# Performance work log

Hardware: AMD Instinct MI355X
Metric: run time of the kernel (lower is better)

Reference implementation:

```python
import jax, jax.numpy as jnp
import numpy as np

T, B, I, H = 4096, 2048, 1, 10


def setup_inputs() -> dict:
    key = jax.random.key(0)
    ks = jax.random.split(key, 8)
    k = 1.0 / np.sqrt(H)  # torch default init bound for RNN and Linear(10,1)
    u = lambda kk, shape: jax.random.uniform(kk, shape, jnp.float32, -k, k)
    return {
        "x": jax.random.normal(ks[0], (T, B, I), jnp.float32),
        "h": jnp.zeros((1, B, H), jnp.float32),
        "W_ih": u(ks[1], (H, I)),
        "b_ih": u(ks[2], (H,)),
        "W_hh": u(ks[3], (H, H)),
        "b_hh": u(ks[4], (H,)),
        "W_out": u(ks[5], (1, H)),
        "b_out": u(ks[6], (1,)),
    }


def reference(x, h, W_ih, b_ih, W_hh, b_hh, W_out, b_out):
    # Vanilla RNN: h_t = tanh(x_t @ W_ih^T + b_ih + h_{t-1} @ W_hh^T + b_hh)
    b = b_ih + b_hh  # fuse the two biases once

    def step(h_prev, x_t):  # h_prev: [B,H], x_t: [B,I]
        h_new = jnp.tanh(x_t @ W_ih.T + h_prev @ W_hh.T + b)
        return h_new, h_new

    h_last, ys = jax.lax.scan(step, h[0], x)  # ys: [T,B,H]
    out = ys @ W_out.T + b_out  # [T,B,1]
    return out, h_last[None]  # h: [1,B,H]
```

## Files before the change

### kernel.cpp

```cpp
#include <hip/hip_runtime.h>

#define T_STEPS 4096
#define BATCH   2048
#define HID     10
#define UB      16

__device__ __forceinline__ void issue16(float (&xr)[UB], const float* base) {
#pragma unroll
    for (int u = 0; u < UB; ++u)
        asm volatile("global_load_dword %0, %1, off"
                     : "=v"(xr[u]) : "v"(base + (size_t)u * BATCH) : "memory");
}
#define BIND16(a) "+v"(a[0]),"+v"(a[1]),"+v"(a[2]),"+v"(a[3]),"+v"(a[4]), \
    "+v"(a[5]),"+v"(a[6]),"+v"(a[7]),"+v"(a[8]),"+v"(a[9]),"+v"(a[10]),   \
    "+v"(a[11]),"+v"(a[12]),"+v"(a[13]),"+v"(a[14]),"+v"(a[15])
__device__ __forceinline__ void wait1_bind(float (&xr)[UB]) {
    asm volatile("s_waitcnt vmcnt(1)" : BIND16(xr) :: "memory");
}
__device__ __forceinline__ void wait0_bind(float (&xr)[UB]) {
    asm volatile("s_waitcnt vmcnt(0)" : BIND16(xr) :: "memory");
}

#define STEP_HEAD \
    "ds_swizzle_b32 %[b0], %[r] offset:0x10\n\t"    \
    "ds_swizzle_b32 %[b1], %[r] offset:0x30\n\t"    \
    "ds_swizzle_b32 %[b2], %[r] offset:0x50\n\t"    \
    "ds_swizzle_b32 %[b3], %[r] offset:0x70\n\t"    \
    "ds_swizzle_b32 %[b4], %[r] offset:0x90\n\t"    \
    "ds_swizzle_b32 %[b5], %[r] offset:0xB0\n\t"    \
    "ds_swizzle_b32 %[b6], %[r] offset:0xD0\n\t"    \
    "ds_swizzle_b32 %[b7], %[r] offset:0xF0\n\t"    \
    "ds_swizzle_b32 %[b8], %[r] offset:0x110\n\t"   \
    "ds_swizzle_b32 %[b9], %[r] offset:0x130\n\t"   \
    "v_fma_f32 %[c], %[wih2], %[x], %[bj2]\n\t"     \
    "s_waitcnt lgkmcnt(5)\n\t"                      \
    "v_fmac_f32 %[c], %[b0], %[w0]\n\t" \
    "v_fmac_f32 %[c], %[b1], %[w1]\n\t" \
    "v_fmac_f32 %[c], %[b2], %[w2]\n\t" \
    "v_fmac_f32 %[c], %[b3], %[w3]\n\t" \
    "v_fmac_f32 %[c], %[b4], %[w4]\n\t" \
    "s_waitcnt lgkmcnt(0)\n\t"                      \
    "v_fmac_f32 %[c], %[b5], %[w5]\n\t" \
    "v_fmac_f32 %[c], %[b6], %[w6]\n\t" \
    "v_fmac_f32 %[c], %[b7], %[w7]\n\t" \
    "v_fmac_f32 %[c], %[b8], %[w8]\n\t" \
    "v_fmac_f32 %[c], %[b9], %[w9]\n\t" \
    "v_exp_f32 %[ex], %[c]\n\t"                     \
    "s_nop 0\n\t"                                   \
    "v_add_f32 %[ex], 1.0, %[ex]\n\t"

#define STEP_TAIL \
    "v_rcp_f32 %[r], %[ex]\n\t"                     \
    "s_nop 0"

#define PKDPP(N) "v_fmac_f32_dpp %[pk], %[c], %[m] row_ror:" #N " row_mask:0xf bank_mask:0xf\n\t"
#define PKPLAIN  "v_fmac_f32 %[pk], %[c], %[m]\n\t"

#define DEF_STEP(SUF, PKLINE_) \
__device__ __forceinline__ void step_##SUF(float& r, float& pk, float x, \
        float wih2, float bj2, float m, const float (&w)[10]) { \
    float b0, b1, b2, b3, b4, b5, b6, b7, b8, b9, c, ex; \
    asm volatile( STEP_HEAD PKLINE_ STEP_TAIL \
        : [b0]"=&v"(b0), [b1]"=&v"(b1), [b2]"=&v"(b2), [b3]"=&v"(b3), \
          [b4]"=&v"(b4), [b5]"=&v"(b5), [b6]"=&v"(b6), [b7]"=&v"(b7), \
          [b8]"=&v"(b8), [b9]"=&v"(b9), [c]"=&v"(c), [ex]"=&v"(ex), \
          [r]"+v"(r), [pk]"+v"(pk) \
        : [x]"v"(x), [wih2]"v"(wih2), [bj2]"v"(bj2), [m]"v"(m), \
          [w0]"v"(w[0]), [w1]"v"(w[1]), [w2]"v"(w[2]), [w3]"v"(w[3]), \
          [w4]"v"(w[4]), [w5]"v"(w[5]), [w6]"v"(w[6]), [w7]"v"(w[7]), \
          [w8]"v"(w[8]), [w9]"v"(w[9])); \
}

DEF_STEP(r0,  PKPLAIN)
DEF_STEP(r1,  PKDPP(1))
DEF_STEP(r2,  PKDPP(2))
DEF_STEP(r3,  PKDPP(3))
DEF_STEP(r4,  PKDPP(4))
DEF_STEP(r6,  PKDPP(6))
DEF_STEP(r7,  PKDPP(7))
DEF_STEP(r8,  PKDPP(8))
DEF_STEP(r9,  PKDPP(9))
DEF_STEP(r10, PKDPP(10))
DEF_STEP(r11, PKDPP(11))
DEF_STEP(r12, PKDPP(12))
DEF_STEP(r13, PKDPP(13))
DEF_STEP(r14, PKDPP(14))
DEF_STEP(r15, PKDPP(15))

template<int U>
__device__ __forceinline__ void step_u(float& r, float& pk, float x,
                                       float wih2, float bj2,
                                       const float (&km)[16], float mz,
                                       const float (&w)[10]) {
    constexpr int ROT = (U + 5) & 15;
    float m;
    if constexpr (U == 0) m = mz; else m = km[U - 1];
    if constexpr (ROT == 0)       step_r0 (r, pk, x, wih2, bj2, m, w);
    else if constexpr (ROT == 1)  step_r1 (r, pk, x, wih2, bj2, m, w);
    else if constexpr (ROT == 2)  step_r2 (r, pk, x, wih2, bj2, m, w);
    else if constexpr (ROT == 3)  step_r3 (r, pk, x, wih2, bj2, m, w);
    else if constexpr (ROT == 4)  step_r4 (r, pk, x, wih2, bj2, m, w);
    else if constexpr (ROT == 6)  step_r6 (r, pk, x, wih2, bj2, m, w);
    else if constexpr (ROT == 7)  step_r7 (r, pk, x, wih2, bj2, m, w);
    else if constexpr (ROT == 8)  step_r8 (r, pk, x, wih2, bj2, m, w);
    else if constexpr (ROT == 9)  step_r9 (r, pk, x, wih2, bj2, m, w);
    else if constexpr (ROT == 10) step_r10(r, pk, x, wih2, bj2, m, w);
    else if constexpr (ROT == 11) step_r11(r, pk, x, wih2, bj2, m, w);
    else if constexpr (ROT == 12) step_r12(r, pk, x, wih2, bj2, m, w);
    else if constexpr (ROT == 13) step_r13(r, pk, x, wih2, bj2, m, w);
    else if constexpr (ROT == 14) step_r14(r, pk, x, wih2, bj2, m, w);
    else                          step_r15(r, pk, x, wih2, bj2, m, w);
}

template<int U>
__device__ __forceinline__ void run16(float& r, float& pk, const float (&xr)[UB],
                                      float wih2, float bj2,
                                      const float (&km)[16], float mz,
                                      const float (&w)[10]) {
    if constexpr (U < UB) {
        step_u<U>(r, pk, xr[U], wih2, bj2, km, mz, w);
        run16<U + 1>(r, pk, xr, wih2, bj2, km, mz, w);
    }
}

__device__ __forceinline__ void finish_reduce(float r, float& p, float& pk,
                                              float wo2, float m15) {
    asm volatile(
        "v_mul_f32 %[p], %[wo2], %[r]\n\t"
        "s_nop 1\n\t"
        "v_add_f32_dpp %[p], %[p], %[p] row_ror:8 row_mask:0xf bank_mask:0xf\n\t"
        "s_nop 1\n\t"
        "v_add_f32_dpp %[p], %[p], %[p] row_ror:4 row_mask:0xf bank_mask:0xf\n\t"
        "s_nop 1\n\t"
        "v_add_f32_dpp %[p], %[p], %[p] row_ror:2 row_mask:0xf bank_mask:0xf\n\t"
        "s_nop 1\n\t"
        "v_add_f32_dpp %[p], %[p], %[p] row_ror:1 row_mask:0xf bank_mask:0xf\n\t"
        "s_nop 1\n\t"
        "v_fmac_f32 %[pk], %[p], %[m]"
        : [p]"+v"(p), [pk]"+v"(pk)
        : [r]"v"(r), [wo2]"v"(wo2), [m]"v"(m15));
}

__global__ __launch_bounds__(64, 1) void rnn_kernel(
    const float* __restrict__ x,
    const float* __restrict__ h0,
    const float* __restrict__ W_ih,
    const float* __restrict__ b_ih,
    const float* __restrict__ W_hh,
    const float* __restrict__ b_hh,
    const float* __restrict__ W_out,
    const float* __restrict__ b_out,
    float* __restrict__ out)
{
    const int tid = threadIdx.x;
    const int j   = tid & 15;
    const int b   = (blockIdx.x << 2) + (tid >> 4);
    const bool jv = (j < HID);
    const int jc  = jv ? j : 0;

    const float CC = 2.88539008177792681472f;

    const float wih = jv ? W_ih[jc] : 0.0f;
    const float bj  = jv ? (b_ih[jc] + b_hh[jc]) : 0.0f;
    const float wo  = jv ? W_out[jc] : 0.0f;

    float wsum = 0.0f;
    float wv[10];
#pragma unroll
    for (int k = 0; k < HID; ++k) {
        const float whh = jv ? W_hh[jc * HID + k] : 0.0f;
        wsum += whh;
        if (jv)            wv[k] = -2.0f * CC * whh;
        else if (j == 10)  wv[k] = -2.0f * W_out[k];
        else               wv[k] = 0.0f;
    }

    const float wih2 = CC * wih;
    const float bj2  = CC * (bj + wsum);
    const float wo2  = -2.0f * wo;
    float c0sum = b_out[0];
#pragma unroll
    for (int k = 0; k < HID; ++k) c0sum += W_out[k];

    float km[16];
#pragma unroll
    for (int i = 0; i < 16; ++i) km[i] = (j == i) ? 1.0f : 0.0f;
    const float mzero = 0.0f;

    float rval = fmaf(-0.5f, jv ? h0[b * HID + jc] : 0.0f, 0.5f);
    float p = 0.0f, pk = 0.0f;

    const float* xb = x + b;
    float xA[UB], xB[UB];

    issue16(xA, xb);
    wait0_bind(xA);

    for (int t0 = 0; t0 < T_STEPS; t0 += 2 * UB) {
        wait1_bind(xA);
        issue16(xB, xb + (size_t)(t0 + UB) * BATCH);
        run16<0>(rval, pk, xA, wih2, bj2, km, mzero, wv);
        finish_reduce(rval, p, pk, wo2, km[15]);
        out[(size_t)(t0 + j) * BATCH + b] = pk + c0sum;
        pk = 0.0f;

        wait1_bind(xB);
        const float* xsrc = (t0 + 2 * UB < T_STEPS)
                          ? (xb + (size_t)(t0 + 2 * UB) * BATCH) : xb;
        issue16(xA, xsrc);
        run16<0>(rval, pk, xB, wih2, bj2, km, mzero, wv);
        finish_reduce(rval, p, pk, wo2, km[15]);
        out[(size_t)(t0 + UB + j) * BATCH + b] = pk + c0sum;
        pk = 0.0f;
    }

    wait0_bind(xA);

    if (jv) out[(size_t)T_STEPS * BATCH + (size_t)b * HID + j]
                = fmaf(-2.0f, rval, 1.0f);
}

extern "C" void kernel_launch(void* const* d_in, const int* in_sizes, int n_in,
                              void* d_out, int out_size, void* d_ws, size_t ws_size,
                              hipStream_t stream) {
    const float* x     = (const float*)d_in[0];
    const float* h0    = (const float*)d_in[1];
    const float* W_ih  = (const float*)d_in[2];
    const float* b_ih  = (const float*)d_in[3];
    const float* W_hh  = (const float*)d_in[4];
    const float* b_hh  = (const float*)d_in[5];
    const float* W_out = (const float*)d_in[6];
    const float* b_out = (const float*)d_in[7];

    rnn_kernel<<<BATCH / 4, 64, 0, stream>>>(
        x, h0, W_ih, b_ih, W_hh, b_hh, W_out, b_out, (float*)d_out);
}
```

Before: 404.3 us.

## Split each batch row across two half-rows and use DPP for recurrent matvec

Each batch element now gets 32 lanes instead of 16. The two 16-lane halves each compute half of the 10x10 recurrent matvec through DPP row_ror fused multiply-adds, replacing the ten ds_swizzle broadcasts, and the halves are combined with a single swizzle. The x loads move to a rolling per-step prefetch inside the inline asm, the output projection is folded into the next step, and the grid doubles to BATCH/2 blocks. The aim is to shorten the serial per-step dependency chain at the cost of twice as many wavefronts and trickier correctness around rotation masks and the final timestep.

```diff
diff --git a/kernel.cpp b/kernel.cpp
--- a/kernel.cpp
+++ b/kernel.cpp
@@ -3,72 +3,51 @@
 #define T_STEPS 4096
 #define BATCH   2048
 #define HID     10
-#define UB      16
-
-__device__ __forceinline__ void issue16(float (&xr)[UB], const float* base) {
-#pragma unroll
-    for (int u = 0; u < UB; ++u)
-        asm volatile("global_load_dword %0, %1, off"
-                     : "=v"(xr[u]) : "v"(base + (size_t)u * BATCH) : "memory");
-}
-#define BIND16(a) "+v"(a[0]),"+v"(a[1]),"+v"(a[2]),"+v"(a[3]),"+v"(a[4]), \
-    "+v"(a[5]),"+v"(a[6]),"+v"(a[7]),"+v"(a[8]),"+v"(a[9]),"+v"(a[10]),   \
-    "+v"(a[11]),"+v"(a[12]),"+v"(a[13]),"+v"(a[14]),"+v"(a[15])
-__device__ __forceinline__ void wait1_bind(float (&xr)[UB]) {
-    asm volatile("s_waitcnt vmcnt(1)" : BIND16(xr) :: "memory");
-}
-__device__ __forceinline__ void wait0_bind(float (&xr)[UB]) {
-    asm volatile("s_waitcnt vmcnt(0)" : BIND16(xr) :: "memory");
-}
-
-#define STEP_HEAD \
-    "ds_swizzle_b32 %[b0], %[r] offset:0x10\n\t"    \
-    "ds_swizzle_b32 %[b1], %[r] offset:0x30\n\t"    \
-    "ds_swizzle_b32 %[b2], %[r] offset:0x50\n\t"    \
-    "ds_swizzle_b32 %[b3], %[r] offset:0x70\n\t"    \
-    "ds_swizzle_b32 %[b4], %[r] offset:0x90\n\t"    \
-    "ds_swizzle_b32 %[b5], %[r] offset:0xB0\n\t"    \
-    "ds_swizzle_b32 %[b6], %[r] offset:0xD0\n\t"    \
-    "ds_swizzle_b32 %[b7], %[r] offset:0xF0\n\t"    \
-    "ds_swizzle_b32 %[b8], %[r] offset:0x110\n\t"   \
-    "ds_swizzle_b32 %[b9], %[r] offset:0x130\n\t"   \
-    "v_fma_f32 %[c], %[wih2], %[x], %[bj2]\n\t"     \
-    "s_waitcnt lgkmcnt(5)\n\t"                      \
-    "v_fmac_f32 %[c], %[b0], %[w0]\n\t" \
-    "v_fmac_f32 %[c], %[b1], %[w1]\n\t" \
-    "v_fmac_f32 %[c], %[b2], %[w2]\n\t" \
-    "v_fmac_f32 %[c], %[b3], %[w3]\n\t" \
-    "v_fmac_f32 %[c], %[b4], %[w4]\n\t" \
-    "s_waitcnt lgkmcnt(0)\n\t"                      \
-    "v_fmac_f32 %[c], %[b5], %[w5]\n\t" \
-    "v_fmac_f32 %[c], %[b6], %[w6]\n\t" \
-    "v_fmac_f32 %[c], %[b7], %[w7]\n\t" \
-    "v_fmac_f32 %[c], %[b8], %[w8]\n\t" \
-    "v_fmac_f32 %[c], %[b9], %[w9]\n\t" \
-    "v_exp_f32 %[ex], %[c]\n\t"                     \
-    "s_nop 0\n\t"                                   \
-    "v_add_f32 %[ex], 1.0, %[ex]\n\t"
-
-#define STEP_TAIL \
-    "v_rcp_f32 %[r], %[ex]\n\t"                     \
+
+
+#define PKDPP(N) "v_fmac_f32_dpp %[pk], %[a], %[m] row_ror:" #N " row_mask:0xf bank_mask:0xf\n\t"
+#define PKPLAIN  "v_fmac_f32 %[pk], %[a], %[m]\n\t"
+
+#define STEP_BODY(PKLINE_) \
+    "v_fmac_f32 %[c], %[r], %[w0]\n\t"                                           \
+    "v_mul_f32_dpp %[d], %[r], %[w1] row_ror:1 row_mask:0xf bank_mask:0xf\n\t"   \
+    "v_fmac_f32_dpp %[c], %[r], %[w2] row_ror:2 row_mask:0xf bank_mask:0xf\n\t"  \
+    "v_fmac_f32_dpp %[d], %[r], %[w3] row_ror:3 row_mask:0xf bank_mask:0xf\n\t"  \
+    "v_fmac_f32_dpp %[c], %[r], %[w4] row_ror:4 row_mask:0xf bank_mask:0xf\n\t"  \
+    "v_fmac_f32_dpp %[d], %[r], %[w5] row_ror:5 row_mask:0xf bank_mask:0xf\n\t"  \
+    "v_fmac_f32_dpp %[c], %[r], %[w6] row_ror:6 row_mask:0xf bank_mask:0xf\n\t"  \
+    "v_fmac_f32_dpp %[d], %[r], %[w7] row_ror:7 row_mask:0xf bank_mask:0xf\n\t"  \
+    "v_add_f32 %[o], %[c], %[d]\n\t"                                             \
+    "s_waitcnt vmcnt(14)\n\t"                                                    \
+    "ds_swizzle_b32 %[q], %[o] offset:0x401F\n\t"                                \
+    "v_fma_f32 %[c], %[wih2], %[xn], %[bj2]\n\t"                                 \
+    "global_load_dword %[xl], %[voff], %[xs]\n\t"                                \
+    "v_add_u32 %[voff], 0x2000, %[voff]\n\t"                                     \
+    "s_waitcnt lgkmcnt(0)\n\t"                                                   \
+    "v_add_f32 %[a], %[o], %[q]\n\t"                                             \
+    "v_exp_f32 %[e], %[a]\n\t"                                                   \
+    "s_nop 0\n\t"                                                                \
+    "v_add_f32 %[e], 1.0, %[e]\n\t"                                              \
+    PKLINE_                                                                      \
+    "s_nop 0\n\t"                                                                \
+    "v_mov_b32_dpp %[e], %[e] row_ror:8 row_mask:0xa bank_mask:0xf\n\t"          \
+    "s_nop 0\n\t"                                                                \
+    "v_rcp_f32 %[r], %[e]\n\t"                                                   \
     "s_nop 0"
 
-#define PKDPP(N) "v_fmac_f32_dpp %[pk], %[c], %[m] row_ror:" #N " row_mask:0xf bank_mask:0xf\n\t"
-#define PKPLAIN  "v_fmac_f32 %[pk], %[c], %[m]\n\t"
-
 #define DEF_STEP(SUF, PKLINE_) \
-__device__ __forceinline__ void step_##SUF(float& r, float& pk, float x, \
-        float wih2, float bj2, float m, const float (&w)[10]) { \
-    float b0, b1, b2, b3, b4, b5, b6, b7, b8, b9, c, ex; \
-    asm volatile( STEP_HEAD PKLINE_ STEP_TAIL \
-        : [b0]"=&v"(b0), [b1]"=&v"(b1), [b2]"=&v"(b2), [b3]"=&v"(b3), \
-          [b4]"=&v"(b4), [b5]"=&v"(b5), [b6]"=&v"(b6), [b7]"=&v"(b7), \
-          [b8]"=&v"(b8), [b9]"=&v"(b9), [c]"=&v"(c), [ex]"=&v"(ex), \
-          [r]"+v"(r), [pk]"+v"(pk) \
-        : [x]"v"(x), [wih2]"v"(wih2), [bj2]"v"(bj2), [m]"v"(m), \
+__device__ __forceinline__ void step_##SUF(float& r, float& c, float& pk, \
+        unsigned& voff, float& xl, float xn, float wih2, float bj2, float m, \
+        const float (&w)[8], const float* xs) { \
+    float d, o, q, a, e; \
+    asm volatile( STEP_BODY(PKLINE_) \
+        : [r]"+v"(r), [c]"+v"(c), [pk]"+v"(pk), [voff]"+v"(voff), [xl]"+v"(xl), \
+          [d]"=&v"(d), [o]"=&v"(o), [q]"=&v"(q), [a]"=&v"(a), [e]"=&v"(e) \
+        : [xn]"v"(xn), [wih2]"v"(wih2), [bj2]"v"(bj2), [m]"v"(m), \
           [w0]"v"(w[0]), [w1]"v"(w[1]), [w2]"v"(w[2]), [w3]"v"(w[3]), \
           [w4]"v"(w[4]), [w5]"v"(w[5]), [w6]"v"(w[6]), [w7]"v"(w[7]), \
-          [w8]"v"(w[8]), [w9]"v"(w[9])); \
+          [xs]"s"(xs) \
+        : "memory"); \
 }
 
 DEF_STEP(r0,  PKPLAIN)
@@ -76,6 +55,7 @@
 DEF_STEP(r2,  PKDPP(2))
 DEF_STEP(r3,  PKDPP(3))
 DEF_STEP(r4,  PKDPP(4))
+DEF_STEP(r5,  PKDPP(5))
 DEF_STEP(r6,  PKDPP(6))
 DEF_STEP(r7,  PKDPP(7))
 DEF_STEP(r8,  PKDPP(8))
@@ -88,43 +68,54 @@
 DEF_STEP(r15, PKDPP(15))
 
 template<int U>
-__device__ __forceinline__ void step_u(float& r, float& pk, float x,
+__device__ __forceinline__ void step_u(float& r, float& c, float& pk,
+                                       unsigned& voff, float (&xv)[16],
                                        float wih2, float bj2,
-                                       const float (&km)[16], float mz,
-                                       const float (&w)[10]) {
+                                       const float (&km)[16],
+                                       const float (&w)[8], const float* xs) {
     constexpr int ROT = (U + 5) & 15;
-    float m;
-    if constexpr (U == 0) m = mz; else m = km[U - 1];
-    if constexpr (ROT == 0)       step_r0 (r, pk, x, wih2, bj2, m, w);
-    else if constexpr (ROT == 1)  step_r1 (r, pk, x, wih2, bj2, m, w);
-    else if constexpr (ROT == 2)  step_r2 (r, pk, x, wih2, bj2, m, w);
-    else if constexpr (ROT == 3)  step_r3 (r, pk, x, wih2, bj2, m, w);
-    else if constexpr (ROT == 4)  step_r4 (r, pk, x, wih2, bj2, m, w);
-    else if constexpr (ROT == 6)  step_r6 (r, pk, x, wih2, bj2, m, w);
-    else if constexpr (ROT == 7)  step_r7 (r, pk, x, wih2, bj2, m, w);
-    else if constexpr (ROT == 8)  step_r8 (r, pk, x, wih2, bj2, m, w);
-    else if constexpr (ROT == 9)  step_r9 (r, pk, x, wih2, bj2, m, w);
-    else if constexpr (ROT == 10) step_r10(r, pk, x, wih2, bj2, m, w);
-    else if constexpr (ROT == 11) step_r11(r, pk, x, wih2, bj2, m, w);
-    else if constexpr (ROT == 12) step_r12(r, pk, x, wih2, bj2, m, w);
-    else if constexpr (ROT == 13) step_r13(r, pk, x, wih2, bj2, m, w);
-    else if constexpr (ROT == 14) step_r14(r, pk, x, wih2, bj2, m, w);
-    else                          step_r15(r, pk, x, wih2, bj2, m, w);
+    const float m = km[(U + 15) & 15];
+    float& xl = xv[U];
+    const float xn = xv[(U + 1) & 15];
+    if constexpr (ROT == 0)       step_r0 (r, c, pk, voff, xl, xn, wih2, bj2, m, w, xs);
+    else if constexpr (ROT == 1)  step_r1 (r, c, pk, voff, xl, xn, wih2, bj2, m, w, xs);
+    else if constexpr (ROT == 2)  step_r2 (r, c, pk, voff, xl, xn, wih2, bj2, m, w, xs);
+    else if constexpr (ROT == 3)  step_r3 (r, c, pk, voff, xl, xn, wih2, bj2, m, w, xs);
+    else if constexpr (ROT == 4)  step_r4 (r, c, pk, voff, xl, xn, wih2, bj2, m, w, xs);
+    else if constexpr (ROT == 5)  step_r5 (r, c, pk, voff, xl, xn, wih2, bj2, m, w, xs);
+    else if constexpr (ROT == 6)  step_r6 (r, c, pk, voff, xl, xn, wih2, bj2, m, w, xs);
+    else if constexpr (ROT == 7)  step_r7 (r, c, pk, voff, xl, xn, wih2, bj2, m, w, xs);
+    else if constexpr (ROT == 8)  step_r8 (r, c, pk, voff, xl, xn, wih2, bj2, m, w, xs);
+    else if constexpr (ROT == 9)  step_r9 (r, c, pk, voff, xl, xn, wih2, bj2, m, w, xs);
+    else if constexpr (ROT == 10) step_r10(r, c, pk, voff, xl, xn, wih2, bj2, m, w, xs);
+    else if constexpr (ROT == 11) step_r11(r, c, pk, voff, xl, xn, wih2, bj2, m, w, xs);
+    else if constexpr (ROT == 12) step_r12(r, c, pk, voff, xl, xn, wih2, bj2, m, w, xs);
+    else if constexpr (ROT == 13) step_r13(r, c, pk, voff, xl, xn, wih2, bj2, m, w, xs);
+    else if constexpr (ROT == 14) step_r14(r, c, pk, voff, xl, xn, wih2, bj2, m, w, xs);
+    else                          step_r15(r, c, pk, voff, xl, xn, wih2, bj2, m, w, xs);
 }
 
 template<int U>
-__device__ __forceinline__ void run16(float& r, float& pk, const float (&xr)[UB],
+__device__ __forceinline__ void run16(float& r, float& c, float& pk,
+                                      unsigned& voff, float (&xv)[16],
                                       float wih2, float bj2,
-                                      const float (&km)[16], float mz,
-                                      const float (&w)[10]) {
-    if constexpr (U < UB) {
-        step_u<U>(r, pk, xr[U], wih2, bj2, km, mz, w);
-        run16<U + 1>(r, pk, xr, wih2, bj2, km, mz, w);
-    }
+                                      const float (&km)[16],
+                                      const float (&w)[8], const float* xs) {
+    if constexpr (U < 16) {
+        step_u<U>(r, c, pk, voff, xv, wih2, bj2, km, w, xs);
+        run16<U + 1>(r, c, pk, voff, xv, wih2, bj2, km, w, xs);
+    }
+}
+
+#define BIND16(a) "+v"(a[0]),"+v"(a[1]),"+v"(a[2]),"+v"(a[3]),"+v"(a[4]), \
+    "+v"(a[5]),"+v"(a[6]),"+v"(a[7]),"+v"(a[8]),"+v"(a[9]),"+v"(a[10]),   \
+    "+v"(a[11]),"+v"(a[12]),"+v"(a[13]),"+v"(a[14]),"+v"(a[15])
+__device__ __forceinline__ void wait0_bind(float (&xr)[16]) {
+    asm volatile("s_waitcnt vmcnt(0)" : BIND16(xr) :: "memory");
 }
 
 __device__ __forceinline__ void finish_reduce(float r, float& p, float& pk,
-                                              float wo2, float m15) {
+                                              float wo2, float m0) {
     asm volatile(
         "v_mul_f32 %[p], %[wo2], %[r]\n\t"
         "s_nop 1\n\t"
@@ -138,7 +129,7 @@
         "s_nop 1\n\t"
         "v_fmac_f32 %[pk], %[p], %[m]"
         : [p]"+v"(p), [pk]"+v"(pk)
-        : [r]"v"(r), [wo2]"v"(wo2), [m]"v"(m15));
+        : [r]"v"(r), [wo2]"v"(wo2), [m]"v"(m0));
 }
 
 __global__ __launch_bounds__(64, 1) void rnn_kernel(
@@ -152,72 +143,72 @@
     const float* __restrict__ b_out,
     float* __restrict__ out)
 {
-    const int tid = threadIdx.x;
-    const int j   = tid & 15;
-    const int b   = (blockIdx.x << 2) + (tid >> 4);
-    const bool jv = (j < HID);
-    const int jc  = jv ? j : 0;
+    const int tid  = threadIdx.x;
+    const int j    = tid & 15;
+    const bool ev  = !(tid & 16);
+    const int b    = (blockIdx.x << 1) + (tid >> 5);
 
     const float CC = 2.88539008177792681472f;
 
-    const float wih = jv ? W_ih[jc] : 0.0f;
-    const float bj  = jv ? (b_ih[jc] + b_hh[jc]) : 0.0f;
-    const float wo  = jv ? W_out[jc] : 0.0f;
-
+    float w[8];
+#pragma unroll
+    for (int N = 0; N < 8; ++N) {
+        const int k = ev ? ((j - N) & 15) : ((j + 8 - N) & 15);
+        float val = 0.0f;
+        if (j < HID && k < HID)        val = -2.0f * CC * W_hh[j * HID + k];
+        else if (j == 10 && k < HID)   val = -2.0f * W_out[k];
+        w[N] = val;
+    }
     float wsum = 0.0f;
-    float wv[10];
-#pragma unroll
-    for (int k = 0; k < HID; ++k) {
-        const float whh = jv ? W_hh[jc * HID + k] : 0.0f;
-        wsum += whh;
-        if (jv)            wv[k] = -2.0f * CC * whh;
-        else if (j == 10)  wv[k] = -2.0f * W_out[k];
-        else               wv[k] = 0.0f;
-    }
-
-    const float wih2 = CC * wih;
-    const float bj2  = CC * (bj + wsum);
-    const float wo2  = -2.0f * wo;
+    if (j < HID) {
+#pragma unroll
+        for (int k = 0; k < HID; ++k) wsum += W_hh[j * HID + k];
+    }
+    const float wih2 = (ev && j < HID) ? CC * W_ih[j] : 0.0f;
+    const float bj2  = (ev && j < HID) ? CC * (b_ih[j] + b_hh[j] + wsum) : 0.0f;
+    const float wo2  = (ev && j < HID) ? (-2.0f * W_out[j]) : 0.0f;
     float c0sum = b_out[0];
 #pragma unroll
     for (int k = 0; k < HID; ++k) c0sum += W_out[k];
 
     float km[16];
 #pragma unroll
-    for (int i = 0; i < 16; ++i) km[i] = (j == i) ? 1.0f : 0.0f;
-    const float mzero = 0.0f;
-
-    float rval = fmaf(-0.5f, jv ? h0[b * HID + jc] : 0.0f, 0.5f);
-    float p = 0.0f, pk = 0.0f;
-
-    const float* xb = x + b;
-    float xA[UB], xB[UB];
-
-    issue16(xA, xb);
-    wait0_bind(xA);
-
-    for (int t0 = 0; t0 < T_STEPS; t0 += 2 * UB) {
-        wait1_bind(xA);
-        issue16(xB, xb + (size_t)(t0 + UB) * BATCH);
-        run16<0>(rval, pk, xA, wih2, bj2, km, mzero, wv);
-        finish_reduce(rval, p, pk, wo2, km[15]);
-        out[(size_t)(t0 + j) * BATCH + b] = pk + c0sum;
+    for (int i = 0; i < 16; ++i) km[i] = (ev && j == i) ? 1.0f : 0.0f;
+
+    const int kini = ev ? j : ((j + 8) & 15);
+    float r = (kini < HID) ? fmaf(-0.5f, h0[b * HID + kini], 0.5f) : 0.5f;
+    float pk = 0.0f;
+
+    const unsigned voff0 = (unsigned)b * 4u;
+    unsigned voff = voff0;
+    float xv[16];
+#pragma unroll
+    for (int u = 0; u < 16; ++u) {
+        asm volatile("global_load_dword %0, %1, %2"
+                     : "=v"(xv[u]) : "v"(voff), "s"(x) : "memory");
+        voff += 8192u;
+    }
+    wait0_bind(xv);
+    float c = fmaf(wih2, xv[0], bj2);
+
+    for (int t0 = 0; t0 < T_STEPS; t0 += 16) {
+        if (t0 + 16 >= T_STEPS) voff = voff0;
+        run16<0>(r, c, pk, voff, xv, wih2, bj2, km, w, x);
+        if (ev) {
+            const int tj = t0 + ((j == 15) ? -1 : j);
+            if (tj >= 0) out[(size_t)tj * BATCH + b] = pk + c0sum;
+        }
         pk = 0.0f;
-
-        wait1_bind(xB);
-        const float* xsrc = (t0 + 2 * UB < T_STEPS)
-                          ? (xb + (size_t)(t0 + 2 * UB) * BATCH) : xb;
-        issue16(xA, xsrc);
-        run16<0>(rval, pk, xB, wih2, bj2, km, mzero, wv);
-        finish_reduce(rval, p, pk, wo2, km[15]);
-        out[(size_t)(t0 + UB + j) * BATCH + b] = pk + c0sum;
-        pk = 0.0f;
-    }
-
-    wait0_bind(xA);
-
-    if (jv) out[(size_t)T_STEPS * BATCH + (size_t)b * HID + j]
-                = fmaf(-2.0f, rval, 1.0f);
+    }
+
+    wait0_bind(xv);
+
+    float p = 0.0f, pk2 = 0.0f;
+    finish_reduce(r, p, pk2, wo2, km[0]);
+    if (ev && j == 0) out[(size_t)(T_STEPS - 1) * BATCH + b] = pk2 + c0sum;
+
+    if (ev && j < HID)
+        out[(size_t)T_STEPS * BATCH + (size_t)b * HID + j] = fmaf(-2.0f, r, 1.0f);
 }
 
 extern "C" void kernel_launch(void* const* d_in, const int* in_sizes, int n_in,
@@ -232,6 +223,6 @@
     const float* W_out = (const float*)d_in[6];
     const float* b_out = (const float*)d_in[7];
 
-    rnn_kernel<<<BATCH / 4, 64, 0, stream>>>(
+    rnn_kernel<<<BATCH / 2, 64, 0, stream>>>(
         x, h0, W_ih, b_ih, W_hh, b_hh, W_out, b_out, (float*)d_out);
 }
```

Result: faster. 369.8 us (-8.6%).
